# Kernel tuning notes

Measured on AMD Instinct MI355X. Metric: run time of the kernel, lower is better.

The kernel has to match this reference:

```python
import jax, jax.numpy as jnp
import numpy as np

N_NODES = 50000
N_EDGES = 800000
FEATURES = 256
HEADS = 8
HEAD_DIM = FEATURES // HEADS
LAYERS = 3
NEG_SLOPE_ATTN = 0.2   # DGL GATConv default negative_slope
NEG_SLOPE_ACT = 0.01   # F.leaky_relu default used as inter-layer activation


def setup_inputs() -> dict:
    key = jax.random.key(0)
    ks = jax.random.split(key, 7)
    x = jax.random.normal(ks[0], (N_NODES, FEATURES), dtype=jnp.float32)
    src = jax.random.randint(ks[1], (N_EDGES,), 0, N_NODES, dtype=jnp.int32)
    dst = jax.random.randint(ks[2], (N_EDGES,), 0, N_NODES, dtype=jnp.int32)
    # Learned params for LAYERS stacked GATConv layers (xavier-ish scaling)
    W = jax.random.normal(ks[3], (LAYERS, FEATURES, FEATURES), dtype=jnp.float32) / np.sqrt(FEATURES)
    al = jax.random.normal(ks[4], (LAYERS, HEADS, HEAD_DIM), dtype=jnp.float32) * 0.1
    ar = jax.random.normal(ks[5], (LAYERS, HEADS, HEAD_DIM), dtype=jnp.float32) * 0.1
    b = jnp.zeros((LAYERS, FEATURES), dtype=jnp.float32)
    return {"x": x, "src": src, "dst": dst, "W": W, "al": al, "ar": ar, "b": b}


def _gat_layer(x, W, al, ar, b, src, dst, apply_act):
    # x: (N, F) -> h: (N, H, D)
    h = (x @ W).reshape(N_NODES, HEADS, HEAD_DIM)
    el = jnp.einsum('nhd,hd->nh', h, al)  # (N, H)
    er = jnp.einsum('nhd,hd->nh', h, ar)  # (N, H)
    # per-edge attention logits, leaky_relu(el[src] + er[dst])
    e = jax.nn.leaky_relu(el[src] + er[dst], negative_slope=NEG_SLOPE_ATTN)  # (E, H)
    # segment softmax over incoming edges of each dst node
    m = jax.ops.segment_max(e, dst, num_segments=N_NODES)   # (N, H)
    ex = jnp.exp(e - m[dst])                                # (E, H)
    s = jax.ops.segment_sum(ex, dst, num_segments=N_NODES)  # (N, H)
    a = ex / s[dst]                                         # (E, H)
    # weighted message aggregation
    msg = h[src] * a[:, :, None]                            # (E, H, D)
    out = jax.ops.segment_sum(msg, dst, num_segments=N_NODES)  # (N, H, D)
    out = out + b.reshape(1, HEADS, HEAD_DIM)
    out = out.reshape(N_NODES, FEATURES)
    if apply_act:
        out = jax.nn.leaky_relu(out, negative_slope=NEG_SLOPE_ACT)
    return out


def reference(x, src, dst, W, al, ar, b):
    for i in range(LAYERS):
        x = _gat_layer(x, W[i], al[i], ar[i], b[i], src, dst, apply_act=(i + 1 < LAYERS))
    # nn.Dropout in eval mode is identity
    return x
```

## Files before the change

### kernel.cpp

```cpp
#include <hip/hip_runtime.h>

#define NN 50000
#define NE 800000
#define F 256
#define NHEADS 8

typedef __attribute__((ext_vector_type(8))) short bf16x8;
typedef __attribute__((ext_vector_type(4))) float f32x4;

__device__ __forceinline__ unsigned short f2bf_rn(float f) {
  unsigned u = __float_as_uint(f);
  u += 0x7fff + ((u >> 16) & 1);
  return (unsigned short)(u >> 16);
}
__device__ __forceinline__ float bf2f(unsigned short b) {
  return __uint_as_float(((unsigned)b) << 16);
}
__device__ __forceinline__ float h2f(unsigned short h) {
  _Float16 f;
  __builtin_memcpy(&f, &h, 2);
  return (float)f;
}
__device__ __forceinline__ unsigned short f2h(float x) {
  _Float16 f = (_Float16)x;
  unsigned short u;
  __builtin_memcpy(&u, &f, 2);
  return u;
}
__device__ __forceinline__ float4 ld_h4(const unsigned short* p) {
  unsigned long long u = *reinterpret_cast<const unsigned long long*>(p);
  return make_float4(h2f((unsigned short)u), h2f((unsigned short)(u >> 16)),
                     h2f((unsigned short)(u >> 32)), h2f((unsigned short)(u >> 48)));
}

__device__ __forceinline__ void gld16(const unsigned short* g, unsigned short* l) {
  __builtin_amdgcn_global_load_lds(
      (const __attribute__((address_space(1))) unsigned int*)g,
      (__attribute__((address_space(3))) unsigned int*)l, 16, 0, 0);
}

__global__ void k_zero_int(int* __restrict__ p, int n) {
  int i = blockIdx.x * blockDim.x + threadIdx.x;
  if (i < n) p[i] = 0;
}

__global__ void k_hist(const int* __restrict__ dst, int* __restrict__ counts, int e) {
  int i = blockIdx.x * blockDim.x + threadIdx.x;
  if (i < e) atomicAdd(&counts[dst[i]], 1);
}

__global__ __launch_bounds__(256) void k_blocksum(const int* __restrict__ counts,
                                                  int* __restrict__ bsum, int n) {
  int i = blockIdx.x * 256 + threadIdx.x;
  int v = (i < n) ? counts[i] : 0;
#pragma unroll
  for (int d = 32; d >= 1; d >>= 1) v += __shfl_xor(v, d, 64);
  __shared__ int sdata[4];
  if ((threadIdx.x & 63) == 0) sdata[threadIdx.x >> 6] = v;
  __syncthreads();
  if (threadIdx.x == 0) bsum[blockIdx.x] = sdata[0] + sdata[1] + sdata[2] + sdata[3];
}

__global__ __launch_bounds__(256) void k_scan_bsums(int* __restrict__ bsum,
                                                    int* __restrict__ off, int nb, int n) {
  __shared__ int buf[256];
  const int tid = threadIdx.x;
  int v = (tid < nb) ? bsum[tid] : 0;
  buf[tid] = v;
  __syncthreads();
  for (int d = 1; d < 256; d <<= 1) {
    int t = (tid >= d) ? buf[tid - d] : 0;
    __syncthreads();
    buf[tid] += t;
    __syncthreads();
  }
  if (tid < nb) bsum[tid] = buf[tid] - v;
  if (tid == 255) off[n] = buf[255];
}

__global__ __launch_bounds__(256) void k_scan_final(int* __restrict__ counts,
                                                    const int* __restrict__ bsum,
                                                    int* __restrict__ off, int n) {
  __shared__ int buf[256];
  const int tid = threadIdx.x;
  const int i = blockIdx.x * 256 + tid;
  int v = (i < n) ? counts[i] : 0;
  buf[tid] = v;
  __syncthreads();
  for (int d = 1; d < 256; d <<= 1) {
    int t = (tid >= d) ? buf[tid - d] : 0;
    __syncthreads();
    buf[tid] += t;
    __syncthreads();
  }
  if (i < n) {
    off[i] = bsum[blockIdx.x] + buf[tid] - v;
    counts[i] = 0;
  }
}

__global__ void k_scatter(const int* __restrict__ src, const int* __restrict__ dst,
                          const int* __restrict__ off, int* __restrict__ cursor,
                          int* __restrict__ csr_src, int e) {
  int i = blockIdx.x * blockDim.x + threadIdx.x;
  if (i < e) {
    int d = dst[i];
    int p = atomicAdd(&cursor[d], 1);
    csr_src[off[d] + p] = src[i];
  }
}

__global__ void k_split(const float* __restrict__ x, unsigned short* __restrict__ hi,
                        unsigned short* __restrict__ lo, int n8) {
  int i = blockIdx.x * blockDim.x + threadIdx.x;
  if (i >= n8) return;
  const float4* xp = reinterpret_cast<const float4*>(x) + (size_t)i * 2;
  float4 a = xp[0], b = xp[1];
  float v[8] = {a.x, a.y, a.z, a.w, b.x, b.y, b.z, b.w};
  unsigned short hv[8], lv[8];
#pragma unroll
  for (int j = 0; j < 8; ++j) {
    hv[j] = f2bf_rn(v[j]);
    lv[j] = f2bf_rn(v[j] - bf2f(hv[j]));
  }
  uint4 ho, lo4;
  ho.x = (unsigned)hv[0] | ((unsigned)hv[1] << 16);
  ho.y = (unsigned)hv[2] | ((unsigned)hv[3] << 16);
  ho.z = (unsigned)hv[4] | ((unsigned)hv[5] << 16);
  ho.w = (unsigned)hv[6] | ((unsigned)hv[7] << 16);
  lo4.x = (unsigned)lv[0] | ((unsigned)lv[1] << 16);
  lo4.y = (unsigned)lv[2] | ((unsigned)lv[3] << 16);
  lo4.z = (unsigned)lv[4] | ((unsigned)lv[5] << 16);
  lo4.w = (unsigned)lv[6] | ((unsigned)lv[7] << 16);
  *reinterpret_cast<uint4*>(&hi[(size_t)i * 8]) = ho;
  *reinterpret_cast<uint4*>(&lo[(size_t)i * 8]) = lo4;
}

__global__ void k_wsplit(const float* __restrict__ W, unsigned short* __restrict__ Whi,
                         unsigned short* __restrict__ Wlo) {
  int i = blockIdx.x * 256 + threadIdx.x;
  int n = i >> 8, k = i & 255;
  float v = W[k * 256 + n];
  unsigned short h = f2bf_rn(v);
  Whi[i] = h;
  Wlo[i] = f2bf_rn(v - bf2f(h));
}

__global__ __launch_bounds__(256) void k_gemm_mfma(
    const unsigned short* __restrict__ Ahi, const unsigned short* __restrict__ Alo,
    const unsigned short* __restrict__ Bhi, const unsigned short* __restrict__ Blo,
    const float* __restrict__ al, const float* __restrict__ ar,
    unsigned short* __restrict__ h2, float* __restrict__ el, float* __restrict__ er,
    int M)
{
  __shared__ unsigned short sAh[128 * 32];
  __shared__ unsigned short sAl[128 * 32];
  __shared__ unsigned short sBh[128 * 32];
  __shared__ unsigned short sBl[128 * 32];
  const int tid = threadIdx.x;
  const int w = tid >> 6, lane = tid & 63;
  const int row0 = blockIdx.x * 128, col0 = blockIdx.y * 128;
  const int wr = w >> 1, wc = w & 1;

  f32x4 acc[4][4];
#pragma unroll
  for (int i = 0; i < 4; ++i)
#pragma unroll
    for (int j = 0; j < 4; ++j) acc[i][j] = (f32x4)0.0f;

  const int l15 = lane & 15;
  const int lq = lane >> 4;
  const int lk = lq * 8;

  for (int step = 0; step < 8; ++step) {
    const int k0 = step * 32;
    __syncthreads();
#pragma unroll
    for (int i = 0; i < 2; ++i) {
      const int u = i * 256 + tid;
      const int r = u >> 2, ku = u & 3;
      const int ubase = (i * 256 + w * 64) * 8;
      const int arow = min(row0 + r, M - 1);
      gld16(Ahi + (size_t)arow * F + k0 + ku * 8, &sAh[ubase]);
      gld16(Alo + (size_t)arow * F + k0 + ku * 8, &sAl[ubase]);
      gld16(Bhi + (size_t)(col0 + r) * F + k0 + ku * 8, &sBh[ubase]);
      gld16(Blo + (size_t)(col0 + r) * F + k0 + ku * 8, &sBl[ubase]);
    }
    __syncthreads();

    bf16x8 ah[4], alv[4], bh[4], bl[4];
#pragma unroll
    for (int f = 0; f < 4; ++f) {
      const int ra = (wr * 64 + f * 16 + l15) * 32 + lk;
      const int rb = (wc * 64 + f * 16 + l15) * 32 + lk;
      ah[f]  = *reinterpret_cast<const bf16x8*>(&sAh[ra]);
      alv[f] = *reinterpret_cast<const bf16x8*>(&sAl[ra]);
      bh[f]  = *reinterpret_cast<const bf16x8*>(&sBh[rb]);
      bl[f]  = *reinterpret_cast<const bf16x8*>(&sBl[rb]);
    }
#pragma unroll
    for (int fr = 0; fr < 4; ++fr)
#pragma unroll
      for (int fc = 0; fc < 4; ++fc) {
        acc[fr][fc] = __builtin_amdgcn_mfma_f32_16x16x32_bf16(ah[fr], bh[fc], acc[fr][fc], 0, 0, 0);
        acc[fr][fc] = __builtin_amdgcn_mfma_f32_16x16x32_bf16(ah[fr], bl[fc], acc[fr][fc], 0, 0, 0);
        acc[fr][fc] = __builtin_amdgcn_mfma_f32_16x16x32_bf16(alv[fr], bh[fc], acc[fr][fc], 0, 0, 0);
      }
  }

#pragma unroll
  for (int fr = 0; fr < 4; ++fr) {
#pragma unroll
    for (int r = 0; r < 4; ++r) {
      const int grow = row0 + wr * 64 + fr * 16 + lq * 4 + r;
      if (grow < M) {
#pragma unroll
        for (int fc = 0; fc < 4; ++fc)
          h2[(size_t)grow * F + col0 + wc * 64 + fc * 16 + l15] = f2h(acc[fr][fc][r]);
      }
    }
  }

  float alc[4], arc[4];
#pragma unroll
  for (int fc = 0; fc < 4; ++fc) {
    const int cg = col0 + wc * 64 + fc * 16 + l15;
    alc[fc] = al[cg];
    arc[fc] = ar[cg];
  }
  const int hb = (col0 + wc * 64) >> 5;
#pragma unroll
  for (int fr = 0; fr < 4; ++fr) {
#pragma unroll
    for (int r = 0; r < 4; ++r) {
      float e0 = acc[fr][0][r] * alc[0] + acc[fr][1][r] * alc[1];
      float e1 = acc[fr][2][r] * alc[2] + acc[fr][3][r] * alc[3];
      float f0 = acc[fr][0][r] * arc[0] + acc[fr][1][r] * arc[1];
      float f1 = acc[fr][2][r] * arc[2] + acc[fr][3][r] * arc[3];
#pragma unroll
      for (int d = 1; d < 16; d <<= 1) {
        e0 += __shfl_xor(e0, d, 64);
        e1 += __shfl_xor(e1, d, 64);
        f0 += __shfl_xor(f0, d, 64);
        f1 += __shfl_xor(f1, d, 64);
      }
      const int n = row0 + wr * 64 + fr * 16 + lq * 4 + r;
      if (l15 == 0 && n < M) {
        el[n * 8 + hb] = e0;
        el[n * 8 + hb + 1] = e1;
        er[n * 8 + hb] = f0;
        er[n * 8 + hb + 1] = f1;
      }
    }
  }
}

__global__ __launch_bounds__(512) void k_agg(
    const unsigned short* __restrict__ h2, const float* __restrict__ el,
    const float* __restrict__ er, const int* __restrict__ off,
    const int* __restrict__ csr_src, const float* __restrict__ bias,
    float* __restrict__ yf, unsigned short* __restrict__ yhi,
    unsigned short* __restrict__ ylo, int mode)
{
  __shared__ float a_lds[8][64][9];
  __shared__ int s_lds[8][64];
  const int wave = threadIdx.x >> 6;
  const int lane = threadIdx.x & 63;
  const int n = blockIdx.x * 8 + wave;
  if (n >= NN) return;
  const int o0 = off[n], o1 = off[n + 1];

  float ern[8];
  {
    const float4 e0 = *reinterpret_cast<const float4*>(&er[n * 8]);
    const float4 e1 = *reinterpret_cast<const float4*>(&er[n * 8 + 4]);
    ern[0] = e0.x; ern[1] = e0.y; ern[2] = e0.z; ern[3] = e0.w;
    ern[4] = e1.x; ern[5] = e1.y; ern[6] = e1.z; ern[7] = e1.w;
  }
  const int c0 = lane * 4;
  const int myh = lane >> 3;
  float asum = 0.f;
  float4 acc0 = make_float4(0.f, 0.f, 0.f, 0.f), acc1 = acc0, acc2 = acc0, acc3 = acc0;

  for (int start = o0; start < o1; start += 64) {
    const int idx = start + lane;
    if (idx < o1) {
      const int s = csr_src[idx];
      s_lds[wave][lane] = s;
      const float4 e0 = *reinterpret_cast<const float4*>(&el[s * 8]);
      const float4 e1 = *reinterpret_cast<const float4*>(&el[s * 8 + 4]);
      float ev[8] = {e0.x, e0.y, e0.z, e0.w, e1.x, e1.y, e1.z, e1.w};
#pragma unroll
      for (int t = 0; t < 8; ++t) {
        float e = ev[t] + ern[t];
        e = e > 0.f ? e : 0.2f * e;
        a_lds[wave][lane][t] = __expf(e);
      }
    }
    asm volatile("s_waitcnt lgkmcnt(0)" ::: "memory");
    __builtin_amdgcn_sched_barrier(0);
    const int cnt = min(64, o1 - start);
    int k = 0;
    for (; k + 8 <= cnt; k += 8) {
      const int s0 = s_lds[wave][k + 0], s1 = s_lds[wave][k + 1];
      const int s2 = s_lds[wave][k + 2], s3 = s_lds[wave][k + 3];
      const int s4 = s_lds[wave][k + 4], s5 = s_lds[wave][k + 5];
      const int s6 = s_lds[wave][k + 6], s7 = s_lds[wave][k + 7];
      const float a0 = a_lds[wave][k + 0][myh], a1 = a_lds[wave][k + 1][myh];
      const float a2 = a_lds[wave][k + 2][myh], a3 = a_lds[wave][k + 3][myh];
      const float a4 = a_lds[wave][k + 4][myh], a5 = a_lds[wave][k + 5][myh];
      const float a6 = a_lds[wave][k + 6][myh], a7 = a_lds[wave][k + 7][myh];
      const float4 h0 = ld_h4(&h2[(size_t)s0 * F + c0]);
      const float4 h1 = ld_h4(&h2[(size_t)s1 * F + c0]);
      const float4 h2v = ld_h4(&h2[(size_t)s2 * F + c0]);
      const float4 h3 = ld_h4(&h2[(size_t)s3 * F + c0]);
      const float4 h4 = ld_h4(&h2[(size_t)s4 * F + c0]);
      const float4 h5 = ld_h4(&h2[(size_t)s5 * F + c0]);
      const float4 h6 = ld_h4(&h2[(size_t)s6 * F + c0]);
      const float4 h7 = ld_h4(&h2[(size_t)s7 * F + c0]);
      asum += ((a0 + a1) + (a2 + a3)) + ((a4 + a5) + (a6 + a7));
      acc0.x = fmaf(a0, h0.x, acc0.x); acc0.y = fmaf(a0, h0.y, acc0.y);
      acc0.z = fmaf(a0, h0.z, acc0.z); acc0.w = fmaf(a0, h0.w, acc0.w);
      acc1.x = fmaf(a1, h1.x, acc1.x); acc1.y = fmaf(a1, h1.y, acc1.y);
      acc1.z = fmaf(a1, h1.z, acc1.z); acc1.w = fmaf(a1, h1.w, acc1.w);
      acc2.x = fmaf(a2, h2v.x, acc2.x); acc2.y = fmaf(a2, h2v.y, acc2.y);
      acc2.z = fmaf(a2, h2v.z, acc2.z); acc2.w = fmaf(a2, h2v.w, acc2.w);
      acc3.x = fmaf(a3, h3.x, acc3.x); acc3.y = fmaf(a3, h3.y, acc3.y);
      acc3.z = fmaf(a3, h3.z, acc3.z); acc3.w = fmaf(a3, h3.w, acc3.w);
      acc0.x = fmaf(a4, h4.x, acc0.x); acc0.y = fmaf(a4, h4.y, acc0.y);
      acc0.z = fmaf(a4, h4.z, acc0.z); acc0.w = fmaf(a4, h4.w, acc0.w);
      acc1.x = fmaf(a5, h5.x, acc1.x); acc1.y = fmaf(a5, h5.y, acc1.y);
      acc1.z = fmaf(a5, h5.z, acc1.z); acc1.w = fmaf(a5, h5.w, acc1.w);
      acc2.x = fmaf(a6, h6.x, acc2.x); acc2.y = fmaf(a6, h6.y, acc2.y);
      acc2.z = fmaf(a6, h6.z, acc2.z); acc2.w = fmaf(a6, h6.w, acc2.w);
      acc3.x = fmaf(a7, h7.x, acc3.x); acc3.y = fmaf(a7, h7.y, acc3.y);
      acc3.z = fmaf(a7, h7.z, acc3.z); acc3.w = fmaf(a7, h7.w, acc3.w);
    }
    for (; k < cnt; ++k) {
      const int s = s_lds[wave][k];
      const float a = a_lds[wave][k][myh];
      const float4 hv = ld_h4(&h2[(size_t)s * F + c0]);
      asum += a;
      acc0.x = fmaf(a, hv.x, acc0.x); acc0.y = fmaf(a, hv.y, acc0.y);
      acc0.z = fmaf(a, hv.z, acc0.z); acc0.w = fmaf(a, hv.w, acc0.w);
    }
    __builtin_amdgcn_sched_barrier(0);
  }

  const float inv = asum > 0.f ? 1.f / asum : 0.f;

  const float4 bv = *reinterpret_cast<const float4*>(&bias[c0]);
  float4 o;
  o.x = (acc0.x + acc1.x + acc2.x + acc3.x) * inv + bv.x;
  o.y = (acc0.y + acc1.y + acc2.y + acc3.y) * inv + bv.y;
  o.z = (acc0.z + acc1.z + acc2.z + acc3.z) * inv + bv.z;
  o.w = (acc0.w + acc1.w + acc2.w + acc3.w) * inv + bv.w;
  if (mode == 0) {
    o.x = o.x > 0.f ? o.x : 0.01f * o.x;
    o.y = o.y > 0.f ? o.y : 0.01f * o.y;
    o.z = o.z > 0.f ? o.z : 0.01f * o.z;
    o.w = o.w > 0.f ? o.w : 0.01f * o.w;
    unsigned short h0 = f2bf_rn(o.x), h1 = f2bf_rn(o.y), h2w = f2bf_rn(o.z), h3 = f2bf_rn(o.w);
    unsigned short l0 = f2bf_rn(o.x - bf2f(h0)), l1 = f2bf_rn(o.y - bf2f(h1));
    unsigned short l2 = f2bf_rn(o.z - bf2f(h2w)), l3 = f2bf_rn(o.w - bf2f(h3));
    uint2 hw, lw;
    hw.x = (unsigned)h0 | ((unsigned)h1 << 16); hw.y = (unsigned)h2w | ((unsigned)h3 << 16);
    lw.x = (unsigned)l0 | ((unsigned)l1 << 16); lw.y = (unsigned)l2 | ((unsigned)l3 << 16);
    *reinterpret_cast<uint2*>(&yhi[(size_t)n * F + c0]) = hw;
    *reinterpret_cast<uint2*>(&ylo[(size_t)n * F + c0]) = lw;
  } else {
    *reinterpret_cast<float4*>(&yf[(size_t)n * F + c0]) = o;
  }
}

extern "C" void kernel_launch(void* const* d_in, const int* in_sizes, int n_in,
                              void* d_out, int out_size, void* d_ws, size_t ws_size,
                              hipStream_t stream) {
  const float* x   = (const float*)d_in[0];
  const int*   src = (const int*)d_in[1];
  const int*   dst = (const int*)d_in[2];
  const float* W   = (const float*)d_in[3];
  const float* al  = (const float*)d_in[4];
  const float* ar  = (const float*)d_in[5];
  const float* b   = (const float*)d_in[6];
  float* out = (float*)d_out;

  char* ws = (char*)d_ws;
  auto take = [&](size_t bytes) {
    char* p = ws;
    ws += (bytes + 255) & ~(size_t)255;
    return p;
  };
  int*   off     = (int*)take((NN + 1) * sizeof(int));
  int*   counts  = (int*)take(NN * sizeof(int));
  int*   bsum    = (int*)take(256 * sizeof(int));
  int*   csr_src = (int*)take(NE * sizeof(int));
  float* el      = (float*)take((size_t)NN * NHEADS * sizeof(float));
  float* er      = (float*)take((size_t)NN * NHEADS * sizeof(float));
  unsigned short* h2    = (unsigned short*)take((size_t)NN * F * 2);
  unsigned short* A_hi  = (unsigned short*)take((size_t)NN * F * 2);
  unsigned short* A_lo  = (unsigned short*)take((size_t)NN * F * 2);
  unsigned short* Wt_hi = (unsigned short*)take((size_t)F * F * 2);
  unsigned short* Wt_lo = (unsigned short*)take((size_t)F * F * 2);

  const int NB = (NN + 255) / 256;
  k_zero_int<<<NB, 256, 0, stream>>>(counts, NN);
  k_hist<<<(NE + 255) / 256, 256, 0, stream>>>(dst, counts, NE);
  k_blocksum<<<NB, 256, 0, stream>>>(counts, bsum, NN);
  k_scan_bsums<<<1, 256, 0, stream>>>(bsum, off, NB, NN);
  k_scan_final<<<NB, 256, 0, stream>>>(counts, bsum, off, NN);
  k_scatter<<<(NE + 255) / 256, 256, 0, stream>>>(src, dst, off, counts, csr_src, NE);

  const int n8 = NN * F / 8;
  k_split<<<(n8 + 255) / 256, 256, 0, stream>>>(x, A_hi, A_lo, n8);
  for (int l = 0; l < 3; ++l) {
    k_wsplit<<<256, 256, 0, stream>>>(W + (size_t)l * F * F, Wt_hi, Wt_lo);
    k_gemm_mfma<<<dim3((NN + 127) / 128, 2), 256, 0, stream>>>(
        A_hi, A_lo, Wt_hi, Wt_lo, al + l * F, ar + l * F, h2, el, er, NN);
    k_agg<<<(NN + 7) / 8, 512, 0, stream>>>(h2, el, er, off, csr_src, b + (size_t)l * F,
                                            out, A_hi, A_lo, (l < 2) ? 0 : 1);
  }
}
```

Measured before the change: 473.5 us.

## Double-buffer A tiles in GEMM, read B from global, remap block order

The GEMM now double-buffers only the A tiles in shared memory and prefetches the next K-slice while computing the current one. The B (weight) fragments are read straight from global memory and rely on cache. A 1D grid with a swizzled block index pairs the two column blocks of neighbouring row tiles so A rows get reused in L2. This cuts one barrier per step and halves shared-memory traffic, at the cost of uncoalesced direct global loads for B.

```diff
diff --git a/kernel.cpp b/kernel.cpp
--- a/kernel.cpp
+++ b/kernel.cpp
@@ -153,13 +153,16 @@
     unsigned short* __restrict__ h2, float* __restrict__ el, float* __restrict__ er,
     int M)
 {
-  __shared__ unsigned short sAh[128 * 32];
-  __shared__ unsigned short sAl[128 * 32];
-  __shared__ unsigned short sBh[128 * 32];
-  __shared__ unsigned short sBl[128 * 32];
+  const int id = blockIdx.x;
+  const int cblk = (id >> 3) & 1;
+  const int rblk = (id & 7) + 8 * (id >> 4);
+  if (rblk >= (M + 127) / 128) return;
+  const int row0 = rblk * 128, col0 = cblk * 128;
+
+  __shared__ unsigned short sAh[2][128 * 32];
+  __shared__ unsigned short sAl[2][128 * 32];
   const int tid = threadIdx.x;
   const int w = tid >> 6, lane = tid & 63;
-  const int row0 = blockIdx.x * 128, col0 = blockIdx.y * 128;
   const int wr = w >> 1, wc = w & 1;
 
   f32x4 acc[4][4];
@@ -172,31 +175,38 @@
   const int lq = lane >> 4;
   const int lk = lq * 8;
 
-  for (int step = 0; step < 8; ++step) {
-    const int k0 = step * 32;
-    __syncthreads();
+  auto stageA = [&](int b, int k0) {
 #pragma unroll
     for (int i = 0; i < 2; ++i) {
       const int u = i * 256 + tid;
       const int r = u >> 2, ku = u & 3;
       const int ubase = (i * 256 + w * 64) * 8;
       const int arow = min(row0 + r, M - 1);
-      gld16(Ahi + (size_t)arow * F + k0 + ku * 8, &sAh[ubase]);
-      gld16(Alo + (size_t)arow * F + k0 + ku * 8, &sAl[ubase]);
-      gld16(Bhi + (size_t)(col0 + r) * F + k0 + ku * 8, &sBh[ubase]);
-      gld16(Blo + (size_t)(col0 + r) * F + k0 + ku * 8, &sBl[ubase]);
-    }
-    __syncthreads();
-
-    bf16x8 ah[4], alv[4], bh[4], bl[4];
+      gld16(Ahi + (size_t)arow * F + k0 + ku * 8, &sAh[b][ubase]);
+      gld16(Alo + (size_t)arow * F + k0 + ku * 8, &sAl[b][ubase]);
+    }
+  };
+
+  stageA(0, 0);
+  __syncthreads();
+  int buf = 0;
+  for (int step = 0; step < 8; ++step) {
+    const int k0 = step * 32;
+    if (step < 7) stageA(buf ^ 1, k0 + 32);
+
+    bf16x8 bh[4], bl[4];
+#pragma unroll
+    for (int f = 0; f < 4; ++f) {
+      const size_t boff = (size_t)(col0 + wc * 64 + f * 16 + l15) * F + k0 + lk;
+      bh[f] = *reinterpret_cast<const bf16x8*>(&Bhi[boff]);
+      bl[f] = *reinterpret_cast<const bf16x8*>(&Blo[boff]);
+    }
+    bf16x8 ah[4], alv[4];
 #pragma unroll
     for (int f = 0; f < 4; ++f) {
       const int ra = (wr * 64 + f * 16 + l15) * 32 + lk;
-      const int rb = (wc * 64 + f * 16 + l15) * 32 + lk;
-      ah[f]  = *reinterpret_cast<const bf16x8*>(&sAh[ra]);
-      alv[f] = *reinterpret_cast<const bf16x8*>(&sAl[ra]);
-      bh[f]  = *reinterpret_cast<const bf16x8*>(&sBh[rb]);
-      bl[f]  = *reinterpret_cast<const bf16x8*>(&sBl[rb]);
+      ah[f]  = *reinterpret_cast<const bf16x8*>(&sAh[buf][ra]);
+      alv[f] = *reinterpret_cast<const bf16x8*>(&sAl[buf][ra]);
     }
 #pragma unroll
     for (int fr = 0; fr < 4; ++fr)
@@ -206,6 +216,8 @@
         acc[fr][fc] = __builtin_amdgcn_mfma_f32_16x16x32_bf16(ah[fr], bl[fc], acc[fr][fc], 0, 0, 0);
         acc[fr][fc] = __builtin_amdgcn_mfma_f32_16x16x32_bf16(alv[fr], bh[fc], acc[fr][fc], 0, 0, 0);
       }
+    __syncthreads();
+    buf ^= 1;
   }
 
 #pragma unroll
@@ -413,9 +425,10 @@
 
   const int n8 = NN * F / 8;
   k_split<<<(n8 + 255) / 256, 256, 0, stream>>>(x, A_hi, A_lo, n8);
+  const int ngemm = ((391 + 7) / 8) * 16;
   for (int l = 0; l < 3; ++l) {
     k_wsplit<<<256, 256, 0, stream>>>(W + (size_t)l * F * F, Wt_hi, Wt_lo);
-    k_gemm_mfma<<<dim3((NN + 127) / 128, 2), 256, 0, stream>>>(
+    k_gemm_mfma<<<ngemm, 256, 0, stream>>>(
         A_hi, A_lo, Wt_hi, Wt_lo, al + l * F, ar + l * F, h2, el, er, NN);
     k_agg<<<(NN + 7) / 8, 512, 0, stream>>>(h2, el, er, off, csr_src, b + (size_t)l * F,
                                             out, A_hi, A_lo, (l < 2) ? 0 : 1);
```

Result: slower. 512.1 us (+8.2%).
